# Kernel tuning notes

Hardware: AMD Instinct MI355X
Metric: run time of the kernel (lower is better)

Reference implementation:

```python
import jax, jax.numpy as jnp
import numpy as np

DIM = 768
NUM_HEADS = 8
HEAD_DIM = DIM // NUM_HEADS


def setup_inputs() -> dict:
    key = jax.random.key(0)
    k1, k2, k3, k4, k5 = jax.random.split(key, 5)
    B, C, H, W = 16, DIM, 32, 32
    x = jax.random.normal(k1, (B, C, H, W), dtype=jnp.float32)
    # Conv2d 1x1 weights expressed as [out_ch, in_ch] matrices
    w_qkv = jax.random.normal(k2, (3 * C, C), dtype=jnp.float32) * (C ** -0.5)
    b_qkv = jax.random.normal(k3, (3 * C,), dtype=jnp.float32) * 0.02
    w_proj = jax.random.normal(k4, (C, C), dtype=jnp.float32) * (C ** -0.5)
    b_proj = jax.random.normal(k5, (C,), dtype=jnp.float32) * 0.02
    return {"x": x, "w_qkv": w_qkv, "b_qkv": b_qkv, "w_proj": w_proj, "b_proj": b_proj}


def reference(x, w_qkv, b_qkv, w_proj, b_proj):
    B, C, H, W = x.shape
    N = H * W
    nh, hd = NUM_HEADS, C // NUM_HEADS
    xf = x.astype(jnp.float32).reshape(B, C, N)  # bcn
    # 1x1 conv == channel matmul
    qkv = jnp.einsum('oc,bcn->bon', w_qkv, xf) + b_qkv[None, :, None]
    qkv = qkv.reshape(B, 3, nh, hd, N)
    q, k, v = qkv[:, 0], qkv[:, 1], qkv[:, 2]  # [B, nh, hd, N]
    s = hd ** -0.25  # scale split between q and k as in the original
    attn = jnp.einsum('bhdn,bhdm->bhnm', q * s, k * s)  # [B, nh, N, N]
    attn = attn - jax.lax.stop_gradient(jnp.max(attn, axis=-1, keepdims=True))
    attn = jnp.clip(attn, -88.0, 88.0)
    attn = jax.nn.softmax(attn, axis=-1)
    # dropout is identity in eval mode
    out = jnp.einsum('bhnm,bhdm->bhdn', attn, v)  # [B, nh, hd, N]
    out = out.reshape(B, C, N)
    out = jnp.einsum('oc,bcn->bon', w_proj, out) + b_proj[None, :, None]
    return out.reshape(B, C, H, W).astype(x.dtype)
```

## Files before the change

kernel.cpp:

```cpp
#include <hip/hip_runtime.h>
#include <stdint.h>

typedef __attribute__((ext_vector_type(4))) float f32x4;
typedef __attribute__((ext_vector_type(16))) float f32x16;
typedef __attribute__((ext_vector_type(8))) short bf16x8;

#define SQKV 0.38372606f
#define RM 8.0f

__device__ __forceinline__ unsigned short f2bf(float f) {
  union { float f; unsigned u; } v; v.f = f;
  unsigned r = v.u + 0x7FFFu + ((v.u >> 16) & 1u);
  return (unsigned short)(r >> 16);
}

__device__ __forceinline__ unsigned cvt_pk_bf16(float a, float b) {
  unsigned r;
  asm volatile("v_cvt_pk_bf16_f32 %0, %1, %2" : "=v"(r) : "v"(a), "v"(b));
  return r;
}
__device__ __forceinline__ void permswap(unsigned &a, unsigned &b) {
  asm volatile("v_permlane32_swap_b32 %0, %1" : "+v"(a), "+v"(b));
}

__device__ __forceinline__ void glds16(const unsigned short* g, unsigned short* l) {
  __builtin_amdgcn_global_load_lds(
      (const __attribute__((address_space(1))) void*)g,
      (__attribute__((address_space(3))) void*)l, 16, 0, 0);
}

__global__ __launch_bounds__(256) void k_convert2(const float* __restrict__ s1,
                                                  const float* __restrict__ s2,
                                                  unsigned short* __restrict__ d1,
                                                  int n1_4, int ntot4) {
  int i = blockIdx.x * 256 + threadIdx.x;
  if (i >= ntot4) return;
  const float4 v = (i < n1_4) ? reinterpret_cast<const float4*>(s1)[i]
                              : reinterpret_cast<const float4*>(s2)[i - n1_4];
  ushort4 o;
  o.x = f2bf(v.x); o.y = f2bf(v.y); o.z = f2bf(v.z); o.w = f2bf(v.w);
  reinterpret_cast<ushort4*>(d1)[i] = o;
}

__global__ __launch_bounds__(256) void k_transpose(const float* __restrict__ x,
                                                   unsigned short* __restrict__ xT) {
  __shared__ float tile[32][33];
  const int t = threadIdx.x;
  const int n0 = blockIdx.x * 32, c0 = blockIdx.y * 32, b = blockIdx.z;
  const int lc = t >> 3, ln = (t & 7) * 4;
  const float4 v = *reinterpret_cast<const float4*>(
      x + ((size_t)b * 768 + c0 + lc) * 1024 + n0 + ln);
  tile[lc][ln] = v.x; tile[lc][ln + 1] = v.y;
  tile[lc][ln + 2] = v.z; tile[lc][ln + 3] = v.w;
  __syncthreads();
  const int sn = t >> 3, sc = (t & 7) * 4;
  ushort4 o;
  o.x = f2bf(tile[sc][sn]);     o.y = f2bf(tile[sc + 1][sn]);
  o.z = f2bf(tile[sc + 2][sn]); o.w = f2bf(tile[sc + 3][sn]);
  *reinterpret_cast<ushort4*>(xT + ((size_t)b * 1024 + n0 + sn) * 768 + c0 + sc) = o;
}

__global__ __launch_bounds__(256, 4) void k_gemm_qkv(
    const unsigned short* __restrict__ A,
    const unsigned short* __restrict__ Bx,
    const float* __restrict__ bias,
    unsigned short* __restrict__ qT,
    unsigned short* __restrict__ kT,
    unsigned short* __restrict__ vO) {
  __shared__ unsigned short As[2 * 128 * 32];
  __shared__ unsigned short Bs[2 * 128 * 32];
  const int t = threadIdx.x;
  const int b = blockIdx.y;
  const int tm = blockIdx.x >> 3, tn = blockIdx.x & 7;
  const int lane = t & 63, w = t >> 6, wr = w >> 1, wc = w & 1;

  const int srow = 16 * w + (lane >> 2);
  const int sg = (lane & 3) ^ ((lane >> 3) & 3);
  const int scol = sg << 3;
  const unsigned short* aptr0 = A + (size_t)(tm * 128 + srow) * 768 + scol;
  const unsigned short* aptr1 = aptr0 + (size_t)64 * 768;
  const unsigned short* bptr0 = Bx + (size_t)b * 1024 * 768 + (size_t)(tn * 128 + srow) * 768 + scol;
  const unsigned short* bptr1 = bptr0 + (size_t)64 * 768;
  unsigned short* const lA0 = As + 512 * w;
  unsigned short* const lA1 = As + 2048 + 512 * w;
  unsigned short* const lB0 = Bs + 512 * w;
  unsigned short* const lB1 = Bs + 2048 + 512 * w;

  f32x4 acc[4][4];
#pragma unroll
  for (int mi = 0; mi < 4; ++mi)
#pragma unroll
    for (int ni = 0; ni < 4; ++ni) acc[mi][ni] = (f32x4)0.0f;

  const int rp = ((lane >> 4) ^ ((lane >> 1) & 3)) << 3;
  const unsigned short* rA[4];
  const unsigned short* rB[4];
#pragma unroll
  for (int mi = 0; mi < 4; ++mi)
    rA[mi] = As + (wr * 64 + mi * 16 + (lane & 15)) * 32 + rp;
#pragma unroll
  for (int ni = 0; ni < 4; ++ni)
    rB[ni] = Bs + (wc * 64 + ni * 16 + (lane & 15)) * 32 + rp;

  glds16(aptr0, lA0);
  glds16(aptr1, lA1);
  glds16(bptr0, lB0);
  glds16(bptr1, lB1);
  aptr0 += 32; aptr1 += 32; bptr0 += 32; bptr1 += 32;

  for (int kt = 0; kt < 24; ++kt) {
    const int cur = kt & 1, nxt = (kt & 1) ^ 1;
    __syncthreads();
    if (kt < 23) {
      glds16(aptr0, lA0 + nxt * 4096);
      glds16(aptr1, lA1 + nxt * 4096);
      glds16(bptr0, lB0 + nxt * 4096);
      glds16(bptr1, lB1 + nxt * 4096);
      aptr0 += 32; aptr1 += 32; bptr0 += 32; bptr1 += 32;
    }

    bf16x8 af[4], bfr[4];
#pragma unroll
    for (int mi = 0; mi < 4; ++mi)
      af[mi] = *reinterpret_cast<const bf16x8*>(rA[mi] + cur * 4096);
#pragma unroll
    for (int ni = 0; ni < 4; ++ni)
      bfr[ni] = *reinterpret_cast<const bf16x8*>(rB[ni] + cur * 4096);
#pragma unroll
    for (int mi = 0; mi < 4; ++mi)
#pragma unroll
      for (int ni = 0; ni < 4; ++ni)
        acc[mi][ni] = __builtin_amdgcn_mfma_f32_16x16x32_bf16(af[mi], bfr[ni], acc[mi][ni], 0, 0, 0);
  }

#pragma unroll
  for (int mi = 0; mi < 4; ++mi) {
    const int o0 = tm * 128 + wr * 64 + mi * 16 + ((lane >> 4) << 2);
    const float4 bb = *reinterpret_cast<const float4*>(bias + o0);
    const float sc = (o0 < 1536) ? SQKV : 1.0f;
    const int om = o0 % 768;
    const int hh = om / 96;
    const int d0 = om % 96;
    const int region = o0 / 768;
    const size_t bh = (size_t)(b * 8 + hh);
#pragma unroll
    for (int ni = 0; ni < 4; ++ni) {
      const int nn = tn * 128 + wc * 64 + ni * 16 + (lane & 15);
      ushort4 st;
      st.x = f2bf((acc[mi][ni][0] + bb.x) * sc);
      st.y = f2bf((acc[mi][ni][1] + bb.y) * sc);
      st.z = f2bf((acc[mi][ni][2] + bb.z) * sc);
      st.w = f2bf((acc[mi][ni][3] + bb.w) * sc);
      if (region == 0) {
        *reinterpret_cast<ushort4*>(qT + (bh * 1024 + nn) * 96 + d0) = st;
      } else if (region == 1) {
        *reinterpret_cast<ushort4*>(kT + (bh * 1024 + nn) * 96 + d0) = st;
      } else {
        unsigned short* vp = vO + (bh * 96 + d0) * 1024 + nn;
        vp[0] = st.x; vp[1024] = st.y; vp[2048] = st.z; vp[3072] = st.w;
      }
    }
  }
}

__global__ __launch_bounds__(256, 2) void k_attn3(
    const unsigned short* __restrict__ qT,
    const unsigned short* __restrict__ kT,
    const unsigned short* __restrict__ vO,
    unsigned short* __restrict__ attoutT) {
  __shared__ unsigned short Ks[2][64 * 104];
  __shared__ unsigned short Vs[2][96 * 72];
  __shared__ float redbuf[4][2][32];

  const int t = threadIdx.x, lane = t & 63, wv = t >> 6;
  const int r31 = lane & 31, h = lane >> 5;
  const int sw = (blockIdx.x & 7) * 64 + (blockIdx.x >> 3);
  const int bh = sw >> 2, qt = sw & 3;
  const int b = bh >> 3, hh = bh & 7;
  const int n0 = qt * 256 + wv * 64;

  bf16x8 Qf0[6], Qf1[6];
  {
    const unsigned short* q0 = qT + ((size_t)bh * 1024 + n0 + r31) * 96 + h * 8;
    const unsigned short* q1 = q0 + (size_t)32 * 96;
#pragma unroll
    for (int ks = 0; ks < 6; ++ks) {
      Qf0[ks] = *reinterpret_cast<const bf16x8*>(q0 + ks * 16);
      Qf1[ks] = *reinterpret_cast<const bf16x8*>(q1 + ks * 16);
    }
  }

  const unsigned short* gptr[6];
  unsigned short* lptr[6];
#pragma unroll
  for (int i = 0; i < 6; ++i) {
    if (i < 3) {
      const int cc = t + i * 256;
      const int row = cc / 12, col = (cc % 12) * 8;
      gptr[i] = kT + ((size_t)bh * 1024 + row) * 96 + col;
      lptr[i] = &Ks[0][row * 104 + col];
    } else {
      const int cv = t + (i - 3) * 256;
      const int d = cv >> 3, col = (cv & 7) * 8;
      gptr[i] = vO + ((size_t)bh * 96 + d) * 1024 + col;
      lptr[i] = &Vs[0][d * 72 + col];
    }
  }
  uint4 rg[6];
#pragma unroll
  for (int i = 0; i < 6; ++i) rg[i] = *reinterpret_cast<const uint4*>(gptr[i]);

  f32x16 oac0[3], oac1[3];
#pragma unroll
  for (int dt = 0; dt < 3; ++dt) { oac0[dt] = (f32x16)0.0f; oac1[dt] = (f32x16)0.0f; }
  float run_l0 = 0.0f, run_l1 = 0.0f;

  int cur = 0;
  for (int it = 0; it < 16; ++it, cur ^= 1) {
#pragma unroll
    for (int i = 0; i < 6; ++i)
      *reinterpret_cast<uint4*>(lptr[i] + cur * (i < 3 ? 64 * 104 : 96 * 72)) = rg[i];
    __syncthreads();
    if (it < 15) {
#pragma unroll
      for (int i = 0; i < 6; ++i) {
        gptr[i] += (i < 3) ? 64 * 96 : 64;
        rg[i] = *reinterpret_cast<const uint4*>(gptr[i]);
      }
    }
    const unsigned short* Kb = &Ks[cur][0];
    const unsigned short* Vb = &Vs[cur][0];

    union { bf16x8 v; unsigned u[4]; } pf0, pf1;

    {
      f32x16 sa0 = (f32x16)0.0f, sa1 = (f32x16)0.0f;
      __builtin_amdgcn_s_setprio(1);
#pragma unroll
      for (int ks = 0; ks < 6; ++ks) {
        const bf16x8 k0 = *reinterpret_cast<const bf16x8*>(Kb + r31 * 104 + ks * 16 + h * 8);
        sa0 = __builtin_amdgcn_mfma_f32_32x32x16_bf16(k0, Qf0[ks], sa0, 0, 0, 0);
        sa1 = __builtin_amdgcn_mfma_f32_32x32x16_bf16(k0, Qf1[ks], sa1, 0, 0, 0);
      }
      __builtin_amdgcn_s_setprio(0);

      float t0 = 0.f, t1 = 0.f, u0 = 0.f, u1 = 0.f;
#pragma unroll
      for (int i = 0; i < 16; i += 2) {
        sa0[i]     = __builtin_amdgcn_exp2f(sa0[i] - RM);     t0 += sa0[i];
        sa0[i + 1] = __builtin_amdgcn_exp2f(sa0[i + 1] - RM); t1 += sa0[i + 1];
        sa1[i]     = __builtin_amdgcn_exp2f(sa1[i] - RM);     u0 += sa1[i];
        sa1[i + 1] = __builtin_amdgcn_exp2f(sa1[i + 1] - RM); u1 += sa1[i + 1];
      }
      float ts = t0 + t1, us = u0 + u1;
      ts += __shfl_xor(ts, 32);
      us += __shfl_xor(us, 32);
      run_l0 += ts; run_l1 += us;

#pragma unroll
      for (int kst = 0; kst < 2; ++kst) {
        const int base = kst * 8;
        {
          unsigned X = cvt_pk_bf16(sa0[base + 0], sa0[base + 1]);
          unsigned Y = cvt_pk_bf16(sa0[base + 2], sa0[base + 3]);
          unsigned Z = cvt_pk_bf16(sa0[base + 4], sa0[base + 5]);
          unsigned W = cvt_pk_bf16(sa0[base + 6], sa0[base + 7]);
          permswap(X, Z); permswap(Y, W);
          pf0.u[0] = X; pf0.u[1] = Y; pf0.u[2] = Z; pf0.u[3] = W;
        }
        {
          unsigned X = cvt_pk_bf16(sa1[base + 0], sa1[base + 1]);
          unsigned Y = cvt_pk_bf16(sa1[base + 2], sa1[base + 3]);
          unsigned Z = cvt_pk_bf16(sa1[base + 4], sa1[base + 5]);
          unsigned W = cvt_pk_bf16(sa1[base + 6], sa1[base + 7]);
          permswap(X, Z); permswap(Y, W);
          pf1.u[0] = X; pf1.u[1] = Y; pf1.u[2] = Z; pf1.u[3] = W;
        }
#pragma unroll
        for (int dt = 0; dt < 3; ++dt) {
          const bf16x8 vf = *reinterpret_cast<const bf16x8*>(
              Vb + (dt * 32 + r31) * 72 + kst * 16 + h * 8);
          oac0[dt] = __builtin_amdgcn_mfma_f32_32x32x16_bf16(pf0.v, vf, oac0[dt], 0, 0, 0);
          oac1[dt] = __builtin_amdgcn_mfma_f32_32x32x16_bf16(pf1.v, vf, oac1[dt], 0, 0, 0);
        }
      }
    }

    {
      f32x16 sb0 = (f32x16)0.0f, sb1 = (f32x16)0.0f;
      __builtin_amdgcn_s_setprio(1);
#pragma unroll
      for (int ks = 0; ks < 6; ++ks) {
        const bf16x8 k1 = *reinterpret_cast<const bf16x8*>(Kb + (32 + r31) * 104 + ks * 16 + h * 8);
        sb0 = __builtin_amdgcn_mfma_f32_32x32x16_bf16(k1, Qf0[ks], sb0, 0, 0, 0);
        sb1 = __builtin_amdgcn_mfma_f32_32x32x16_bf16(k1, Qf1[ks], sb1, 0, 0, 0);
      }
      __builtin_amdgcn_s_setprio(0);

      float t0 = 0.f, t1 = 0.f, u0 = 0.f, u1 = 0.f;
#pragma unroll
      for (int i = 0; i < 16; i += 2) {
        sb0[i]     = __builtin_amdgcn_exp2f(sb0[i] - RM);     t0 += sb0[i];
        sb0[i + 1] = __builtin_amdgcn_exp2f(sb0[i + 1] - RM); t1 += sb0[i + 1];
        sb1[i]     = __builtin_amdgcn_exp2f(sb1[i] - RM);     u0 += sb1[i];
        sb1[i + 1] = __builtin_amdgcn_exp2f(sb1[i + 1] - RM); u1 += sb1[i + 1];
      }
      float ts = t0 + t1, us = u0 + u1;
      ts += __shfl_xor(ts, 32);
      us += __shfl_xor(us, 32);
      run_l0 += ts; run_l1 += us;

#pragma unroll
      for (int kst = 2; kst < 4; ++kst) {
        const int base = (kst & 1) * 8;
        {
          unsigned X = cvt_pk_bf16(sb0[base + 0], sb0[base + 1]);
          unsigned Y = cvt_pk_bf16(sb0[base + 2], sb0[base + 3]);
          unsigned Z = cvt_pk_bf16(sb0[base + 4], sb0[base + 5]);
          unsigned W = cvt_pk_bf16(sb0[base + 6], sb0[base + 7]);
          permswap(X, Z); permswap(Y, W);
          pf0.u[0] = X; pf0.u[1] = Y; pf0.u[2] = Z; pf0.u[3] = W;
        }
        {
          unsigned X = cvt_pk_bf16(sb1[base + 0], sb1[base + 1]);
          unsigned Y = cvt_pk_bf16(sb1[base + 2], sb1[base + 3]);
          unsigned Z = cvt_pk_bf16(sb1[base + 4], sb1[base + 5]);
          unsigned W = cvt_pk_bf16(sb1[base + 6], sb1[base + 7]);
          permswap(X, Z); permswap(Y, W);
          pf1.u[0] = X; pf1.u[1] = Y; pf1.u[2] = Z; pf1.u[3] = W;
        }
#pragma unroll
        for (int dt = 0; dt < 3; ++dt) {
          const bf16x8 vf = *reinterpret_cast<const bf16x8*>(
              Vb + (dt * 32 + r31) * 72 + kst * 16 + h * 8);
          oac0[dt] = __builtin_amdgcn_mfma_f32_32x32x16_bf16(pf0.v, vf, oac0[dt], 0, 0, 0);
          oac1[dt] = __builtin_amdgcn_mfma_f32_32x32x16_bf16(pf1.v, vf, oac1[dt], 0, 0, 0);
        }
      }
    }
  }

  if (lane < 32) redbuf[wv][0][lane] = 1.0f / run_l0;
  else           redbuf[wv][1][r31]  = 1.0f / run_l1;
  f32x4 i40[4], i41[4];
#pragma unroll
  for (int q = 0; q < 4; ++q) {
    i40[q] = *reinterpret_cast<const f32x4*>(&redbuf[wv][0][q * 8 + h * 4]);
    i41[q] = *reinterpret_cast<const f32x4*>(&redbuf[wv][1][q * 8 + h * 4]);
  }
  unsigned short* ob0 = attoutT + ((size_t)b * 1024 + n0) * 768 + hh * 96;
  unsigned short* ob1 = ob0 + (size_t)32 * 768;
#pragma unroll
  for (int dt = 0; dt < 3; ++dt)
#pragma unroll
    for (int q = 0; q < 4; ++q)
#pragma unroll
      for (int j = 0; j < 4; ++j) {
        const int np = q * 8 + h * 4 + j;
        ob0[(size_t)np * 768 + dt * 32 + r31] = f2bf(oac0[dt][q * 4 + j] * i40[q][j]);
        ob1[(size_t)np * 768 + dt * 32 + r31] = f2bf(oac1[dt][q * 4 + j] * i41[q][j]);
      }
}

__global__ __launch_bounds__(256, 4) void k_gemm_proj(
    const unsigned short* __restrict__ Aat,
    const unsigned short* __restrict__ Bw,
    const float* __restrict__ bias,
    float* __restrict__ out) {
  __shared__ unsigned short As[2 * 128 * 32];
  __shared__ unsigned short Bs[2 * 128 * 32];
  const int t = threadIdx.x;
  const int b = blockIdx.y;
  const int tm = blockIdx.x / 6, tn = blockIdx.x % 6;
  const int lane = t & 63, w = t >> 6, wr = w >> 1, wc = w & 1;

  const int srow = 16 * w + (lane >> 2);
  const int sg = (lane & 3) ^ ((lane >> 3) & 3);
  const int scol = sg << 3;
  const unsigned short* aptr0 = Aat + (size_t)b * 1024 * 768 + (size_t)(tm * 128 + srow) * 768 + scol;
  const unsigned short* aptr1 = aptr0 + (size_t)64 * 768;
  const unsigned short* bptr0 = Bw + (size_t)(tn * 128 + srow) * 768 + scol;
  const unsigned short* bptr1 = bptr0 + (size_t)64 * 768;
  unsigned short* const lA0 = As + 512 * w;
  unsigned short* const lA1 = As + 2048 + 512 * w;
  unsigned short* const lB0 = Bs + 512 * w;
  unsigned short* const lB1 = Bs + 2048 + 512 * w;

  f32x4 acc[4][4];
#pragma unroll
  for (int mi = 0; mi < 4; ++mi)
#pragma unroll
    for (int ni = 0; ni < 4; ++ni) acc[mi][ni] = (f32x4)0.0f;

  const int rp = ((lane >> 4) ^ ((lane >> 1) & 3)) << 3;
  const unsigned short* rA[4];
  const unsigned short* rB[4];
#pragma unroll
  for (int mi = 0; mi < 4; ++mi)
    rA[mi] = As + (wr * 64 + mi * 16 + (lane & 15)) * 32 + rp;
#pragma unroll
  for (int ni = 0; ni < 4; ++ni)
    rB[ni] = Bs + (wc * 64 + ni * 16 + (lane & 15)) * 32 + rp;

  glds16(aptr0, lA0);
  glds16(aptr1, lA1);
  glds16(bptr0, lB0);
  glds16(bptr1, lB1);
  aptr0 += 32; aptr1 += 32; bptr0 += 32; bptr1 += 32;

  for (int kt = 0; kt < 24; ++kt) {
    const int cur = kt & 1, nxt = (kt & 1) ^ 1;
    __syncthreads();
    if (kt < 23) {
      glds16(aptr0, lA0 + nxt * 4096);
      glds16(aptr1, lA1 + nxt * 4096);
      glds16(bptr0, lB0 + nxt * 4096);
      glds16(bptr1, lB1 + nxt * 4096);
      aptr0 += 32; aptr1 += 32; bptr0 += 32; bptr1 += 32;
    }

    bf16x8 af[4], bfr[4];
#pragma unroll
    for (int mi = 0; mi < 4; ++mi)
      af[mi] = *reinterpret_cast<const bf16x8*>(rA[mi] + cur * 4096);
#pragma unroll
    for (int ni = 0; ni < 4; ++ni)
      bfr[ni] = *reinterpret_cast<const bf16x8*>(rB[ni] + cur * 4096);
#pragma unroll
    for (int mi = 0; mi < 4; ++mi)
#pragma unroll
      for (int ni = 0; ni < 4; ++ni)
        acc[mi][ni] = __builtin_amdgcn_mfma_f32_16x16x32_bf16(af[mi], bfr[ni], acc[mi][ni], 0, 0, 0);
  }

#pragma unroll
  for (int mi = 0; mi < 4; ++mi) {
    const int n0 = tm * 128 + wr * 64 + mi * 16 + ((lane >> 4) << 2);
#pragma unroll
    for (int ni = 0; ni < 4; ++ni) {
      const int o = tn * 128 + wc * 64 + ni * 16 + (lane & 15);
      const float bo = bias[o];
      float4 vv;
      vv.x = acc[mi][ni][0] + bo;
      vv.y = acc[mi][ni][1] + bo;
      vv.z = acc[mi][ni][2] + bo;
      vv.w = acc[mi][ni][3] + bo;
      *reinterpret_cast<float4*>(out + ((size_t)b * 768 + o) * 1024 + n0) = vv;
    }
  }
}

extern "C" void kernel_launch(void* const* d_in, const int* in_sizes, int n_in,
                              void* d_out, int out_size, void* d_ws, size_t ws_size,
                              hipStream_t stream) {
  const float* x = (const float*)d_in[0];
  const float* w_qkv = (const float*)d_in[1];
  const float* b_qkv = (const float*)d_in[2];
  const float* w_proj = (const float*)d_in[3];
  const float* b_proj = (const float*)d_in[4];
  float* out = (float*)d_out;

  unsigned short* ws = (unsigned short*)d_ws;
  unsigned short* wqkv_bf = ws;
  unsigned short* wproj_bf = wqkv_bf + 2304 * 768;
  unsigned short* xT = wproj_bf + 768 * 768;
  unsigned short* qT = xT + (size_t)16 * 1024 * 768;
  unsigned short* kT = qT + (size_t)16 * 8 * 1024 * 96;
  unsigned short* vO = kT + (size_t)16 * 8 * 1024 * 96;
  unsigned short* attoutT = xT;

  const int n1_4 = 2304 * 768 / 4;
  const int ntot4 = n1_4 + 768 * 768 / 4;
  k_convert2<<<(ntot4 + 255) / 256, 256, 0, stream>>>(w_qkv, w_proj, wqkv_bf, n1_4, ntot4);
  k_transpose<<<dim3(32, 24, 16), 256, 0, stream>>>(x, xT);
  k_gemm_qkv<<<dim3(144, 16), 256, 0, stream>>>(wqkv_bf, xT, b_qkv, qT, kT, vO);
  k_attn3<<<512, 256, 0, stream>>>(qT, kT, vO, attoutT);
  k_gemm_proj<<<dim3(48, 16), 256, 0, stream>>>(attoutT, wproj_bf, b_proj, out);
}
```

Measured before the change: 226.7 us.

## Enlarge QKV GEMM tile to 256x128 with triple-buffered async LDS pipeline

The QKV projection GEMM now uses 256x128 output tiles (8x4 MFMA accumulators per wave) on a flattened 1152-block grid. It also replaces the double-buffered loop with a three-stage global-to-LDS prefetch pipeline, synchronised by explicit vmcnt waits and raw barriers. MFMA bursts are wrapped in s_setprio. The aim is more data reuse per LDS load and deeper overlap of memory latency with compute. The cost is more registers and LDS, which lowers occupancy to 2 blocks per CU.

```diff
diff --git a/kernel.cpp b/kernel.cpp
--- a/kernel.cpp
+++ b/kernel.cpp
@@ -60,82 +60,93 @@
   *reinterpret_cast<ushort4*>(xT + ((size_t)b * 1024 + n0 + sn) * 768 + c0 + sc) = o;
 }
 
-__global__ __launch_bounds__(256, 4) void k_gemm_qkv(
+__global__ __launch_bounds__(256, 2) void k_gemm_qkv(
     const unsigned short* __restrict__ A,
     const unsigned short* __restrict__ Bx,
     const float* __restrict__ bias,
     unsigned short* __restrict__ qT,
     unsigned short* __restrict__ kT,
     unsigned short* __restrict__ vO) {
-  __shared__ unsigned short As[2 * 128 * 32];
-  __shared__ unsigned short Bs[2 * 128 * 32];
+  __shared__ unsigned short As[3 * 8192];
+  __shared__ unsigned short Bs[3 * 4096];
   const int t = threadIdx.x;
-  const int b = blockIdx.y;
-  const int tm = blockIdx.x >> 3, tn = blockIdx.x & 7;
-  const int lane = t & 63, w = t >> 6, wr = w >> 1, wc = w & 1;
-
-  const int srow = 16 * w + (lane >> 2);
-  const int sg = (lane & 3) ^ ((lane >> 3) & 3);
-  const int scol = sg << 3;
-  const unsigned short* aptr0 = A + (size_t)(tm * 128 + srow) * 768 + scol;
-  const unsigned short* aptr1 = aptr0 + (size_t)64 * 768;
-  const unsigned short* bptr0 = Bx + (size_t)b * 1024 * 768 + (size_t)(tn * 128 + srow) * 768 + scol;
-  const unsigned short* bptr1 = bptr0 + (size_t)64 * 768;
-  unsigned short* const lA0 = As + 512 * w;
-  unsigned short* const lA1 = As + 2048 + 512 * w;
-  unsigned short* const lB0 = Bs + 512 * w;
-  unsigned short* const lB1 = Bs + 2048 + 512 * w;
-
-  f32x4 acc[4][4];
-#pragma unroll
-  for (int mi = 0; mi < 4; ++mi)
+  const int tm = blockIdx.x >> 7;
+  const int tn = blockIdx.x & 127;
+  const int lane = t & 63, w = t >> 6;
+  const int wm = w >> 1, wn = w & 1;
+  const int w512 = w * 512;
+
+  const int sr = t >> 2;
+  const int sg8 = ((t & 3) ^ ((t >> 3) & 3)) << 3;
+  const unsigned short* aLo = A + (size_t)(tm * 256 + sr) * 768 + sg8;
+  const unsigned short* bLo = Bx + ((size_t)tn * 128 + sr) * 768 + sg8;
+
+  f32x4 acc[8][4];
+#pragma unroll
+  for (int mi = 0; mi < 8; ++mi)
 #pragma unroll
     for (int ni = 0; ni < 4; ++ni) acc[mi][ni] = (f32x4)0.0f;
 
   const int rp = ((lane >> 4) ^ ((lane >> 1) & 3)) << 3;
-  const unsigned short* rA[4];
-  const unsigned short* rB[4];
-#pragma unroll
-  for (int mi = 0; mi < 4; ++mi)
-    rA[mi] = As + (wr * 64 + mi * 16 + (lane & 15)) * 32 + rp;
-#pragma unroll
-  for (int ni = 0; ni < 4; ++ni)
-    rB[ni] = Bs + (wc * 64 + ni * 16 + (lane & 15)) * 32 + rp;
-
-  glds16(aptr0, lA0);
-  glds16(aptr1, lA1);
-  glds16(bptr0, lB0);
-  glds16(bptr1, lB1);
-  aptr0 += 32; aptr1 += 32; bptr0 += 32; bptr1 += 32;
-
+  const int arowoff = (wm * 128 + (lane & 15)) * 32 + rp;
+  const int browoff = (wn * 64 + (lane & 15)) * 32 + rp;
+
+  auto stage = [&](int j, int bf) {
+    const size_t ko = (size_t)j * 32;
+    glds16(aLo + ko,               As + bf * 8192 + w512);
+    glds16(aLo + ko +  64 * 768,   As + bf * 8192 + 2048 + w512);
+    glds16(aLo + ko + 128 * 768,   As + bf * 8192 + 4096 + w512);
+    glds16(aLo + ko + 192 * 768,   As + bf * 8192 + 6144 + w512);
+    glds16(bLo + ko,               Bs + bf * 4096 + w512);
+    glds16(bLo + ko +  64 * 768,   Bs + bf * 4096 + 2048 + w512);
+  };
+
+  stage(0, 0); stage(1, 1); stage(2, 2);
+
+  int buf = 0;
   for (int kt = 0; kt < 24; ++kt) {
-    const int cur = kt & 1, nxt = (kt & 1) ^ 1;
-    __syncthreads();
-    if (kt < 23) {
-      glds16(aptr0, lA0 + nxt * 4096);
-      glds16(aptr1, lA1 + nxt * 4096);
-      glds16(bptr0, lB0 + nxt * 4096);
-      glds16(bptr1, lB1 + nxt * 4096);
-      aptr0 += 32; aptr1 += 32; bptr0 += 32; bptr1 += 32;
-    }
-
-    bf16x8 af[4], bfr[4];
-#pragma unroll
-    for (int mi = 0; mi < 4; ++mi)
-      af[mi] = *reinterpret_cast<const bf16x8*>(rA[mi] + cur * 4096);
+    if (kt < 22)      asm volatile("s_waitcnt vmcnt(12)" ::: "memory");
+    else if (kt == 22) asm volatile("s_waitcnt vmcnt(6)" ::: "memory");
+    else               asm volatile("s_waitcnt vmcnt(0)" ::: "memory");
+    asm volatile("s_barrier" ::: "memory");
+
+    const unsigned short* Ab = As + buf * 8192 + arowoff;
+    const unsigned short* Bb = Bs + buf * 4096 + browoff;
+    bf16x8 bfr[4], af[4];
 #pragma unroll
     for (int ni = 0; ni < 4; ++ni)
-      bfr[ni] = *reinterpret_cast<const bf16x8*>(rB[ni] + cur * 4096);
+      bfr[ni] = *reinterpret_cast<const bf16x8*>(Bb + ni * 512);
+#pragma unroll
+    for (int mi = 0; mi < 4; ++mi)
+      af[mi] = *reinterpret_cast<const bf16x8*>(Ab + mi * 512);
+    __builtin_amdgcn_s_setprio(1);
 #pragma unroll
     for (int mi = 0; mi < 4; ++mi)
 #pragma unroll
       for (int ni = 0; ni < 4; ++ni)
         acc[mi][ni] = __builtin_amdgcn_mfma_f32_16x16x32_bf16(af[mi], bfr[ni], acc[mi][ni], 0, 0, 0);
-  }
-
-#pragma unroll
-  for (int mi = 0; mi < 4; ++mi) {
-    const int o0 = tm * 128 + wr * 64 + mi * 16 + ((lane >> 4) << 2);
+    __builtin_amdgcn_s_setprio(0);
+#pragma unroll
+    for (int mi = 0; mi < 4; ++mi)
+      af[mi] = *reinterpret_cast<const bf16x8*>(Ab + (mi + 4) * 512);
+    __builtin_amdgcn_s_setprio(1);
+#pragma unroll
+    for (int mi = 0; mi < 4; ++mi)
+#pragma unroll
+      for (int ni = 0; ni < 4; ++ni)
+        acc[mi + 4][ni] = __builtin_amdgcn_mfma_f32_16x16x32_bf16(af[mi], bfr[ni], acc[mi + 4][ni], 0, 0, 0);
+    __builtin_amdgcn_s_setprio(0);
+
+    asm volatile("s_waitcnt lgkmcnt(0)" ::: "memory");
+    asm volatile("s_barrier" ::: "memory");
+    if (kt < 21) stage(kt + 3, buf);
+    buf = (buf == 2) ? 0 : buf + 1;
+  }
+
+  const int b = tn >> 3;
+#pragma unroll
+  for (int mi = 0; mi < 8; ++mi) {
+    const int o0 = tm * 256 + wm * 128 + mi * 16 + ((lane >> 4) << 2);
     const float4 bb = *reinterpret_cast<const float4*>(bias + o0);
     const float sc = (o0 < 1536) ? SQKV : 1.0f;
     const int om = o0 % 768;
@@ -145,7 +156,7 @@
     const size_t bh = (size_t)(b * 8 + hh);
 #pragma unroll
     for (int ni = 0; ni < 4; ++ni) {
-      const int nn = tn * 128 + wc * 64 + ni * 16 + (lane & 15);
+      const int nn = (tn & 7) * 128 + wn * 64 + ni * 16 + (lane & 15);
       ushort4 st;
       st.x = f2bf((acc[mi][ni][0] + bb.x) * sc);
       st.y = f2bf((acc[mi][ni][1] + bb.y) * sc);
@@ -473,7 +484,7 @@
   const int ntot4 = n1_4 + 768 * 768 / 4;
   k_convert2<<<(ntot4 + 255) / 256, 256, 0, stream>>>(w_qkv, w_proj, wqkv_bf, n1_4, ntot4);
   k_transpose<<<dim3(32, 24, 16), 256, 0, stream>>>(x, xT);
-  k_gemm_qkv<<<dim3(144, 16), 256, 0, stream>>>(wqkv_bf, xT, b_qkv, qT, kT, vO);
+  k_gemm_qkv<<<1152, 256, 0, stream>>>(wqkv_bf, xT, b_qkv, qT, kT, vO);
   k_attn3<<<512, 256, 0, stream>>>(qT, kT, vO, attoutT);
   k_gemm_proj<<<dim3(48, 16), 256, 0, stream>>>(attoutT, wproj_bf, b_proj, out);
 }
```

Measured after the change: 215.7 us. 1.05x faster.
